# Kernel tuning notes

Hardware: AMD Instinct MI355X
Metric: run time of the kernel (lower is better)

The kernel has to match this reference:

```python
import jax, jax.numpy as jnp
import numpy as np

D_MODEL = 1024
NUM_HEADS = 16
D_HEAD = D_MODEL // NUM_HEADS


def setup_inputs() -> dict:
    key = jax.random.key(0)
    ks = jax.random.split(key, 11)
    B, S = 2, 2048
    s = 1.0 / np.sqrt(D_MODEL)
    inp = {
        "Q": jax.random.normal(ks[0], (B, S, D_MODEL), dtype=jnp.float32),
        "K": jax.random.normal(ks[1], (B, S, D_MODEL), dtype=jnp.float32),
        "V": jax.random.normal(ks[2], (B, S, D_MODEL), dtype=jnp.float32),
        "W_q": jax.random.normal(ks[3], (D_MODEL, D_MODEL), dtype=jnp.float32) * s,
        "b_q": jnp.zeros((D_MODEL,), dtype=jnp.float32),
        "W_k": jax.random.normal(ks[4], (D_MODEL, D_MODEL), dtype=jnp.float32) * s,
        "b_k": jnp.zeros((D_MODEL,), dtype=jnp.float32),
        "W_v": jax.random.normal(ks[5], (D_MODEL, D_MODEL), dtype=jnp.float32) * s,
        "b_v": jnp.zeros((D_MODEL,), dtype=jnp.float32),
        "W_o": jax.random.normal(ks[6], (D_MODEL, D_MODEL), dtype=jnp.float32) * s,
        "b_o": jnp.zeros((D_MODEL,), dtype=jnp.float32),
    }
    return inp


def reference(Q, K, V, W_q, b_q, W_k, b_k, W_v, b_v, W_o, b_o):
    B, S, _ = Q.shape
    # Linear projections (torch Linear: x @ W.T + b)
    q = Q @ W_q.T + b_q  # [B,S,D]
    k = K @ W_k.T + b_k
    v = V @ W_v.T + b_v
    # split heads -> [B,H,S,d]
    q = q.reshape(B, S, NUM_HEADS, D_HEAD).transpose(0, 2, 1, 3)
    k = k.reshape(B, S, NUM_HEADS, D_HEAD).transpose(0, 2, 1, 3)
    v = v.reshape(B, S, NUM_HEADS, D_HEAD).transpose(0, 2, 1, 3)
    scores = jnp.einsum("bhqd,bhkd->bhqk", q, k) / np.sqrt(D_HEAD).astype(np.float32)
    attn = jax.nn.softmax(scores, axis=-1)
    out = jnp.einsum("bhqk,bhkd->bhqd", attn, v)
    out = out.transpose(0, 2, 1, 3).reshape(B, S, D_MODEL)
    return out @ W_o.T + b_o
```

## Files before the change

kernel.cpp:

```cpp
#include <hip/hip_runtime.h>
#include <stdint.h>

#define D_MODEL 1024
#define S_LEN   2048
#define BATCH   2
#define NHEAD   16
#define DHEAD   64
#define NTOK    (BATCH * S_LEN)

typedef unsigned short u16;
typedef __attribute__((ext_vector_type(8))) short bf16x8;
typedef __attribute__((ext_vector_type(4))) float f32x4;
typedef __attribute__((ext_vector_type(16))) float f32x16;
typedef __attribute__((ext_vector_type(2))) unsigned int u32x2;

__device__ __forceinline__ unsigned pack2bf(float lo, float hi) {
    unsigned a = __float_as_uint(lo) + 0x8000u;
    unsigned b = __float_as_uint(hi) + 0x8000u;
    return __builtin_amdgcn_perm(b, a, 0x07060302u);
}
__device__ __forceinline__ u16 f2bf1(float f) {
    return (u16)((__float_as_uint(f) + 0x8000u) >> 16);
}

#define GAS(p) ((const __attribute__((address_space(1))) void*)(p))
#define LAS(p) ((__attribute__((address_space(3))) void*)(p))
#define SWZ8(row, c) (((((row) << 3) | ((c) ^ ((row) & 7)))) << 3)

__global__ __launch_bounds__(256) void convert_kernel(
    const float* __restrict__ Q, const float* __restrict__ K, const float* __restrict__ V,
    const float* __restrict__ Wq, const float* __restrict__ Wk,
    const float* __restrict__ Wv, const float* __restrict__ Wo,
    u16* __restrict__ Qb, u16* __restrict__ Kb, u16* __restrict__ Vb,
    u16* __restrict__ Wqb, u16* __restrict__ Wkb, u16* __restrict__ Wvb, u16* __restrict__ Wob)
{
    const size_t SEG = 262144;
    size_t start = (size_t)blockIdx.x * 4096;
    int s = (int)(start / SEG);
    const float* src; u16* dst; size_t seg0;
    if (s < 4)       { src = Q;  dst = Qb;  seg0 = 0; }
    else if (s < 8)  { src = K;  dst = Kb;  seg0 = 4 * SEG; }
    else if (s < 12) { src = V;  dst = Vb;  seg0 = 8 * SEG; }
    else if (s == 12){ src = Wq; dst = Wqb; seg0 = 12 * SEG; }
    else if (s == 13){ src = Wk; dst = Wkb; seg0 = 13 * SEG; }
    else if (s == 14){ src = Wv; dst = Wvb; seg0 = 14 * SEG; }
    else             { src = Wo; dst = Wob; seg0 = 15 * SEG; }
    size_t off = start - seg0 + threadIdx.x;
    const float4* s4 = (const float4*)src;
    #pragma unroll
    for (int k = 0; k < 16; ++k) {
        float4 x = s4[off + (size_t)k * 256];
        u32x2 p = (u32x2){pack2bf(x.x, x.y), pack2bf(x.z, x.w)};
        *(u32x2*)(dst + (off + (size_t)k * 256) * 4) = p;
    }
}

__global__ __launch_bounds__(512, 2) void proj_kernel(
    const u16* __restrict__ Qb, const u16* __restrict__ Kb, const u16* __restrict__ Vb,
    const u16* __restrict__ Wqb, const u16* __restrict__ Wkb, const u16* __restrict__ Wvb,
    const float* __restrict__ bq, const float* __restrict__ bk, const float* __restrict__ bv,
    u16* __restrict__ qw, u16* __restrict__ kw, u16* __restrict__ vtw)
{
    const int bid = blockIdx.x;
    const int wid = (bid & 7) * 24 + (bid >> 3);
    const int z = wid >> 6;
    const int r = wid & 63;
    const int nbase = (r >> 2) * 256;
    const int mbase = (r & 3) * 256;

    const u16* Ag = (z == 0) ? Wqb : (z == 1) ? Wkb : Wvb;
    const u16* Bg = (z == 0) ? Qb  : (z == 1) ? Kb  : Vb;
    const float* bias = (z == 0) ? bq : (z == 1) ? bk : bv;

    const int tid = threadIdx.x, lane = tid & 63, wave = tid >> 6;
    const int l31 = lane & 31, hh = lane >> 5;
    const int wm = wave >> 2;
    const int wn = wave & 3;

    __shared__ __align__(16) u16 smem[65536];

    size_t aoff[4], boff[4];
    #pragma unroll
    for (int c = 0; c < 4; ++c) {
        int p = (wave * 4 + c) * 64 + lane;
        int row = p >> 3;
        int cg  = (p & 7) ^ (row & 7);
        aoff[c] = (size_t)(mbase + row) * D_MODEL + cg * 8;
        boff[c] = (size_t)(nbase + row) * D_MODEL + cg * 8;
    }

#define STAGE(buf, kc)                                                              \
    do {                                                                            \
        _Pragma("unroll")                                                           \
        for (int c = 0; c < 4; ++c) {                                               \
            __builtin_amdgcn_global_load_lds(GAS(Ag + aoff[c] + (kc)),              \
                LAS(smem + (buf) * 16384 + (wave * 4 + c) * 512), 16, 0, 0);        \
            __builtin_amdgcn_global_load_lds(GAS(Bg + boff[c] + (kc)),              \
                LAS(smem + 32768 + (buf) * 16384 + (wave * 4 + c) * 512), 16, 0, 0);\
        }                                                                           \
    } while (0)

    STAGE(0, 0);

    f32x16 acc[4][2];
    #pragma unroll
    for (int mt = 0; mt < 4; ++mt)
        #pragma unroll
        for (int nt = 0; nt < 2; ++nt)
            #pragma unroll
            for (int q = 0; q < 16; ++q) acc[mt][nt][q] = 0.f;

    for (int t = 0; t < D_MODEL / 64; ++t) {
        const int cur = t & 1;
        asm volatile("s_waitcnt vmcnt(0) lgkmcnt(0)" ::: "memory");
        __builtin_amdgcn_s_barrier();
        asm volatile("" ::: "memory");
        if (t < D_MODEL / 64 - 1) STAGE(cur ^ 1, (t + 1) * 64);
        const u16* Ab = smem + cur * 16384;
        const u16* Bb = smem + 32768 + cur * 16384;
        #pragma unroll
        for (int kk = 0; kk < 4; ++kk) {
            bf16x8 af[4], bfr[2];
            #pragma unroll
            for (int mt = 0; mt < 4; ++mt)
                af[mt] = *(const bf16x8*)&Ab[SWZ8(wm * 128 + mt * 32 + l31, kk * 2 + hh)];
            #pragma unroll
            for (int nt = 0; nt < 2; ++nt)
                bfr[nt] = *(const bf16x8*)&Bb[SWZ8(wn * 64 + nt * 32 + l31, kk * 2 + hh)];
            #pragma unroll
            for (int mt = 0; mt < 4; ++mt)
                #pragma unroll
                for (int nt = 0; nt < 2; ++nt)
                    acc[mt][nt] = __builtin_amdgcn_mfma_f32_32x32x16_bf16(af[mt], bfr[nt], acc[mt][nt], 0, 0, 0);
        }
    }
#undef STAGE

    if (z < 2) {
        u16* Y = z ? kw : qw;
        const float scale = z ? 1.0f : 0.18033688011112042f;
        #pragma unroll
        for (int mt = 0; mt < 4; ++mt)
            #pragma unroll
            for (int nt = 0; nt < 2; ++nt) {
                const int tok = nbase + wn * 64 + nt * 32 + l31;
                u16* yrow = Y + (size_t)tok * D_MODEL;
                #pragma unroll
                for (int g = 0; g < 4; ++g) {
                    const int d0 = mbase + wm * 128 + mt * 32 + 8 * g + 4 * hh;
                    float4 b4 = *(const float4*)&bias[d0];
                    float v0 = (acc[mt][nt][4 * g + 0] + b4.x) * scale;
                    float v1 = (acc[mt][nt][4 * g + 1] + b4.y) * scale;
                    float v2 = (acc[mt][nt][4 * g + 2] + b4.z) * scale;
                    float v3 = (acc[mt][nt][4 * g + 3] + b4.w) * scale;
                    *(u32x2*)(yrow + d0) = (u32x2){pack2bf(v0, v1), pack2bf(v2, v3)};
                }
            }
    } else {
        #pragma unroll
        for (int mt = 0; mt < 4; ++mt)
            #pragma unroll
            for (int nt = 0; nt < 2; ++nt) {
                const int tok = nbase + wn * 64 + nt * 32 + l31;
                #pragma unroll
                for (int g = 0; g < 4; ++g) {
                    const int d0 = mbase + wm * 128 + mt * 32 + 8 * g + 4 * hh;
                    #pragma unroll
                    for (int q = 0; q < 4; ++q)
                        vtw[(size_t)(d0 + q) * NTOK + tok] =
                            f2bf1(acc[mt][nt][4 * g + q] + bias[d0 + q]);
                }
            }
    }
}

__global__ __launch_bounds__(512, 4) void attn_kernel(
    const u16* __restrict__ qw, const u16* __restrict__ kw,
    const u16* __restrict__ vtw, u16* __restrict__ aw)
{
    const int qbase = blockIdx.x * 128;
    const int h = blockIdx.y, b = blockIdx.z;
    const int tid = threadIdx.x, lane = tid & 63, wave = tid >> 6;
    const int wq = wave & 3;
    const int wk = wave >> 2;
    const int l31 = lane & 31;
    const int hh  = lane >> 5;
    const int colbase = h * DHEAD;
    const size_t qrow0 = (size_t)b * S_LEN + qbase;

    __shared__ __align__(16) u16 smem[17664];
    #define KS_OFF(buf) ((buf) * 4096)
    #define VS_OFF(buf) (8192 + (buf) * 4096)

    const int srow = tid >> 3;
    const int scg  = (tid & 7) ^ (srow & 7);
    const size_t ksrc = ((size_t)b * S_LEN + srow) * D_MODEL + colbase + scg * 8;
    const size_t vsrc = (size_t)(colbase + srow) * NTOK + (size_t)b * S_LEN + scg * 8;

    #define STAGE_KV(buf, kv0)                                                         \
        do {                                                                           \
            __builtin_amdgcn_global_load_lds(GAS(kw + ksrc + (size_t)(kv0) * D_MODEL), \
                                             LAS(smem + KS_OFF(buf) + wave * 512), 16, 0, 0); \
            __builtin_amdgcn_global_load_lds(GAS(vtw + vsrc + (kv0)),                  \
                                             LAS(smem + VS_OFF(buf) + wave * 512), 16, 0, 0); \
        } while (0)

    bf16x8 qf[4];
    {
        const u16* qptr = qw + (qrow0 + wq * 32 + l31) * D_MODEL + colbase + hh * 8;
        #pragma unroll
        for (int s = 0; s < 4; ++s) qf[s] = *(const bf16x8*)(qptr + s * 16);
    }

    STAGE_KV(0, 0);

    f32x16 o[2];
    #pragma unroll
    for (int dt = 0; dt < 2; ++dt)
        #pragma unroll
        for (int r = 0; r < 16; ++r) o[dt][r] = 0.f;
    float l = 0.f;

    __syncthreads();

    for (int t = 0; t < S_LEN / 64; ++t) {
        const int cur = t & 1;
        if (t + 1 < S_LEN / 64) STAGE_KV(!cur, (t + 1) * 64);

        f32x16 sc;
        #pragma unroll
        for (int r = 0; r < 16; ++r) sc[r] = -12.f;
        __builtin_amdgcn_s_setprio(1);
        #pragma unroll
        for (int s = 0; s < 4; ++s) {
            bf16x8 kf = *(const bf16x8*)&smem[KS_OFF(cur) + SWZ8(wk * 32 + l31, s * 2 + hh)];
            sc = __builtin_amdgcn_mfma_f32_32x32x16_bf16(kf, qf[s], sc, 0, 0, 0);
        }
        __builtin_amdgcn_s_setprio(0);

        unsigned x[4][2];
        #pragma unroll
        for (int g = 0; g < 4; ++g) {
            float p0 = __builtin_amdgcn_exp2f(sc[4 * g + 0]);
            float p1 = __builtin_amdgcn_exp2f(sc[4 * g + 1]);
            float p2 = __builtin_amdgcn_exp2f(sc[4 * g + 2]);
            float p3 = __builtin_amdgcn_exp2f(sc[4 * g + 3]);
            l += (p0 + p1) + (p2 + p3);
            asm("v_cvt_pk_bf16_f32 %0, %1, %2" : "=v"(x[g][0]) : "v"(p0), "v"(p1));
            asm("v_cvt_pk_bf16_f32 %0, %1, %2" : "=v"(x[g][1]) : "v"(p2), "v"(p3));
        }

        #pragma unroll
        for (int sp = 0; sp < 2; ++sp) {
            unsigned a0 = x[2 * sp][0], b0 = x[2 * sp + 1][0];
            unsigned a1 = x[2 * sp][1], b1 = x[2 * sp + 1][1];
            asm("v_permlane32_swap_b32 %0, %1" : "+v"(a0), "+v"(b0));
            asm("v_permlane32_swap_b32 %0, %1" : "+v"(a1), "+v"(b1));
            union { unsigned u[4]; bf16x8 v; } pf;
            pf.u[0] = a0; pf.u[1] = a1; pf.u[2] = b0; pf.u[3] = b1;
            __builtin_amdgcn_s_setprio(1);
            #pragma unroll
            for (int dt = 0; dt < 2; ++dt) {
                bf16x8 vf = *(const bf16x8*)&smem[VS_OFF(cur) + SWZ8(dt * 32 + l31, wk * 4 + sp * 2 + hh)];
                o[dt] = __builtin_amdgcn_mfma_f32_32x32x16_bf16(vf, pf.v, o[dt], 0, 0, 0);
            }
            __builtin_amdgcn_s_setprio(0);
        }

        __syncthreads();
    }

    l += __shfl_xor(l, 32);

    float* Ored = (float*)smem;
    float* Lred = (float*)(smem + 17408);
    float* op = Ored + ((size_t)wq * 32 + l31) * 68;
    if (wk == 1) {
        #pragma unroll
        for (int dt = 0; dt < 2; ++dt)
            #pragma unroll
            for (int g = 0; g < 4; ++g)
                *(f32x4*)(op + dt * 32 + 8 * g + 4 * hh) =
                    (f32x4){o[dt][4 * g + 0], o[dt][4 * g + 1], o[dt][4 * g + 2], o[dt][4 * g + 3]};
        if (hh == 0) Lred[wq * 32 + l31] = l;
    }
    __syncthreads();
    if (wk == 0) {
        l += Lred[wq * 32 + l31];
        float inv = 1.0f / l;
        size_t orow = (qrow0 + wq * 32 + l31) * D_MODEL + colbase;
        #pragma unroll
        for (int dt = 0; dt < 2; ++dt)
            #pragma unroll
            for (int g = 0; g < 4; ++g) {
                f32x4 add = *(const f32x4*)(op + dt * 32 + 8 * g + 4 * hh);
                float v0 = (o[dt][4 * g + 0] + add[0]) * inv;
                float v1 = (o[dt][4 * g + 1] + add[1]) * inv;
                float v2 = (o[dt][4 * g + 2] + add[2]) * inv;
                float v3 = (o[dt][4 * g + 3] + add[3]) * inv;
                *(u32x2*)(aw + orow + dt * 32 + 8 * g + 4 * hh) =
                    (u32x2){pack2bf(v0, v1), pack2bf(v2, v3)};
            }
    }
    #undef STAGE_KV
    #undef KS_OFF
    #undef VS_OFF
}

__global__ __launch_bounds__(256) void outproj_kernel(
    const u16* __restrict__ aw, const u16* __restrict__ Wob,
    const float* __restrict__ bo, float* __restrict__ out)
{
    const int nbase = blockIdx.x * 64;
    const int mbase = blockIdx.y * 128;
    const int tid = threadIdx.x, lane = tid & 63, wave = tid >> 6;
    const int m16 = lane & 15, quad = lane >> 4;
    const int wm = wave >> 1, wn = wave & 1;

    __shared__ __align__(16) u16 As[128 * 64];
    __shared__ __align__(16) u16 Bs[64 * 64];

    int arow[4], acg[4], brow[2], bcg[2];
    #pragma unroll
    for (int c = 0; c < 4; ++c) {
        int p = (wave * 4 + c) * 64 + lane;
        arow[c] = p >> 3; acg[c] = (p & 7) ^ (arow[c] & 7);
    }
    #pragma unroll
    for (int c = 0; c < 2; ++c) {
        int p = (wave * 2 + c) * 64 + lane;
        brow[c] = p >> 3; bcg[c] = (p & 7) ^ (brow[c] & 7);
    }

    f32x4 acc[4][2];
    #pragma unroll
    for (int mt = 0; mt < 4; ++mt)
        #pragma unroll
        for (int nt = 0; nt < 2; ++nt) acc[mt][nt] = (f32x4){0.f, 0.f, 0.f, 0.f};

    for (int kc = 0; kc < D_MODEL; kc += 64) {
        #pragma unroll
        for (int c = 0; c < 4; ++c)
            __builtin_amdgcn_global_load_lds(
                GAS(Wob + (size_t)(mbase + arow[c]) * D_MODEL + kc + acg[c] * 8),
                LAS(As + (wave * 4 + c) * 512), 16, 0, 0);
        #pragma unroll
        for (int c = 0; c < 2; ++c)
            __builtin_amdgcn_global_load_lds(
                GAS(aw + (size_t)(nbase + brow[c]) * D_MODEL + kc + bcg[c] * 8),
                LAS(Bs + (wave * 2 + c) * 512), 16, 0, 0);
        __syncthreads();
        #pragma unroll
        for (int half = 0; half < 2; ++half) {
            bf16x8 af[4], bfr[2];
            #pragma unroll
            for (int mt = 0; mt < 4; ++mt)
                af[mt] = *(const bf16x8*)&As[SWZ8(wm * 64 + mt * 16 + m16, quad + 4 * half)];
            #pragma unroll
            for (int nt = 0; nt < 2; ++nt)
                bfr[nt] = *(const bf16x8*)&Bs[SWZ8(wn * 32 + nt * 16 + m16, quad + 4 * half)];
            #pragma unroll
            for (int mt = 0; mt < 4; ++mt)
                #pragma unroll
                for (int nt = 0; nt < 2; ++nt)
                    acc[mt][nt] = __builtin_amdgcn_mfma_f32_16x16x32_bf16(af[mt], bfr[nt], acc[mt][nt], 0, 0, 0);
        }
        __syncthreads();
    }

    #pragma unroll
    for (int mt = 0; mt < 4; ++mt) {
        int d0 = mbase + wm * 64 + mt * 16 + quad * 4;
        float4 b4 = *(const float4*)&bo[d0];
        #pragma unroll
        for (int nt = 0; nt < 2; ++nt) {
            int tok = nbase + wn * 32 + nt * 16 + m16;
            float4 st;
            st.x = acc[mt][nt][0] + b4.x;
            st.y = acc[mt][nt][1] + b4.y;
            st.z = acc[mt][nt][2] + b4.z;
            st.w = acc[mt][nt][3] + b4.w;
            *(float4*)(out + (size_t)tok * D_MODEL + d0) = st;
        }
    }
}

extern "C" void kernel_launch(void* const* d_in, const int* in_sizes, int n_in,
                              void* d_out, int out_size, void* d_ws, size_t ws_size,
                              hipStream_t stream) {
    const float* Q  = (const float*)d_in[0];
    const float* K  = (const float*)d_in[1];
    const float* V  = (const float*)d_in[2];
    const float* Wq = (const float*)d_in[3];
    const float* bq = (const float*)d_in[4];
    const float* Wk = (const float*)d_in[5];
    const float* bk = (const float*)d_in[6];
    const float* Wv = (const float*)d_in[7];
    const float* bv = (const float*)d_in[8];
    const float* Wo = (const float*)d_in[9];
    const float* bo = (const float*)d_in[10];

    const size_t NT = (size_t)NTOK * D_MODEL;
    const size_t WN = (size_t)D_MODEL * D_MODEL;
    u16* base = (u16*)d_ws;
    u16* qw  = base;
    u16* kw  = base + NT;
    u16* vtw = base + 2 * NT;
    u16* Qb  = base + 3 * NT;
    u16* Kb  = base + 4 * NT;
    u16* Vb  = base + 5 * NT;
    u16* Wqb = base + 6 * NT;
    u16* Wkb = Wqb + WN;
    u16* Wvb = Wkb + WN;
    u16* Wob = Wvb + WN;
    u16* aww = Qb;

    convert_kernel<<<1024, 256, 0, stream>>>(Q, K, V, Wq, Wk, Wv, Wo,
                                             Qb, Kb, Vb, Wqb, Wkb, Wvb, Wob);
    proj_kernel<<<dim3(192), 512, 0, stream>>>(Qb, Kb, Vb, Wqb, Wkb, Wvb,
                                               bq, bk, bv, qw, kw, vtw);
    attn_kernel<<<dim3(S_LEN / 128, NHEAD, BATCH), 512, 0, stream>>>(qw, kw, vtw, aww);
    outproj_kernel<<<dim3(NTOK / 64, D_MODEL / 128), 256, 0, stream>>>(
        aww, Wob, bo, (float*)d_out);
}
```

Before: 214.0 us.

## Restructure projection GEMM main loop into barrier-synchronized quadrant phases with MFMA priority

The projection GEMM's K-loop now splits each 64-wide k-tile into four quadrant phases. Each phase loads A/B fragments from LDS for all four k-steps and then runs MFMAs on a 2x1 sub-block of the accumulator tile. Barriers around each MFMA burst and s_setprio(1) are meant to interleave waves so one wave's LDS reads overlap another's MFMA work, ping-pong style. The prefetch of the next tile is issued in the first phase and waited on only in the last, which keeps global loads in flight longer. The cost is two extra workgroup barriers per phase and more fragment registers, so occupancy could drop.

```diff
diff --git a/kernel.cpp b/kernel.cpp
--- a/kernel.cpp
+++ b/kernel.cpp
@@ -110,28 +110,38 @@
             #pragma unroll
             for (int q = 0; q < 16; ++q) acc[mt][nt][q] = 0.f;
 
-    for (int t = 0; t < D_MODEL / 64; ++t) {
+    asm volatile("s_waitcnt vmcnt(0)" ::: "memory");
+    __builtin_amdgcn_s_barrier();
+    asm volatile("" ::: "memory");
+
+    for (int t = 0; t < 16; ++t) {
         const int cur = t & 1;
-        asm volatile("s_waitcnt vmcnt(0) lgkmcnt(0)" ::: "memory");
-        __builtin_amdgcn_s_barrier();
-        asm volatile("" ::: "memory");
-        if (t < D_MODEL / 64 - 1) STAGE(cur ^ 1, (t + 1) * 64);
         const u16* Ab = smem + cur * 16384;
         const u16* Bb = smem + 32768 + cur * 16384;
         #pragma unroll
-        for (int kk = 0; kk < 4; ++kk) {
-            bf16x8 af[4], bfr[2];
-            #pragma unroll
-            for (int mt = 0; mt < 4; ++mt)
-                af[mt] = *(const bf16x8*)&Ab[SWZ8(wm * 128 + mt * 32 + l31, kk * 2 + hh)];
-            #pragma unroll
-            for (int nt = 0; nt < 2; ++nt)
-                bfr[nt] = *(const bf16x8*)&Bb[SWZ8(wn * 64 + nt * 32 + l31, kk * 2 + hh)];
-            #pragma unroll
-            for (int mt = 0; mt < 4; ++mt)
-                #pragma unroll
-                for (int nt = 0; nt < 2; ++nt)
-                    acc[mt][nt] = __builtin_amdgcn_mfma_f32_32x32x16_bf16(af[mt], bfr[nt], acc[mt][nt], 0, 0, 0);
+        for (int q = 0; q < 4; ++q) {
+            const int qm = q >> 1, qn = q & 1;
+            if (q == 0 && t < 15) STAGE(cur ^ 1, (t + 1) * 64);
+            bf16x8 af0[4], af1[4], bfr[4];
+            #pragma unroll
+            for (int kk = 0; kk < 4; ++kk) {
+                af0[kk] = *(const bf16x8*)&Ab[SWZ8(wm * 128 + (2 * qm) * 32 + l31, kk * 2 + hh)];
+                af1[kk] = *(const bf16x8*)&Ab[SWZ8(wm * 128 + (2 * qm + 1) * 32 + l31, kk * 2 + hh)];
+                bfr[kk] = *(const bf16x8*)&Bb[SWZ8(wn * 64 + qn * 32 + l31, kk * 2 + hh)];
+            }
+            if (q == 3 && t < 15) asm volatile("s_waitcnt vmcnt(0)" ::: "memory");
+            asm volatile("" ::: "memory");
+            __builtin_amdgcn_s_barrier();
+            asm volatile("s_waitcnt lgkmcnt(0)" ::: "memory");
+            __builtin_amdgcn_s_setprio(1);
+            #pragma unroll
+            for (int kk = 0; kk < 4; ++kk) {
+                acc[2 * qm][qn]     = __builtin_amdgcn_mfma_f32_32x32x16_bf16(af0[kk], bfr[kk], acc[2 * qm][qn], 0, 0, 0);
+                acc[2 * qm + 1][qn] = __builtin_amdgcn_mfma_f32_32x32x16_bf16(af1[kk], bfr[kk], acc[2 * qm + 1][qn], 0, 0, 0);
+            }
+            __builtin_amdgcn_s_setprio(0);
+            asm volatile("" ::: "memory");
+            __builtin_amdgcn_s_barrier();
         }
     }
 #undef STAGE
```

Result: slower. 226.2 us (+5.7%).

## Rework output projection into double-buffered 128x128 tiles using 32x32 MFMA

Applied to the files above, without the earlier changes.

The output-projection GEMM now uses 128x128 tiles with 512 threads and 256 blocks remapped in a swizzled order. Global-to-LDS loads are double-buffered so the next K chunk is fetched while the current one is computed. The inner product switches from 16x16x32 to 32x32x16 MFMA instructions with raised scheduling priority. The aim is to hide load latency, raise data reuse per block and cut barriers, at the cost of fewer blocks and more LDS per block.

```diff
diff --git a/kernel.cpp b/kernel.cpp
--- a/kernel.cpp
+++ b/kernel.cpp
@@ -307,82 +307,90 @@
     #undef VS_OFF
 }
 
-__global__ __launch_bounds__(256) void outproj_kernel(
+__global__ __launch_bounds__(512, 2) void outproj_kernel(
     const u16* __restrict__ aw, const u16* __restrict__ Wob,
     const float* __restrict__ bo, float* __restrict__ out)
 {
-    const int nbase = blockIdx.x * 64;
-    const int mbase = blockIdx.y * 128;
+    const int bid = blockIdx.x;
+    const int wid = (bid & 7) * 32 + (bid >> 3);
+    const int mbase = (wid & 7) * 128;
+    const int nbase = (wid >> 3) * 128;
+
     const int tid = threadIdx.x, lane = tid & 63, wave = tid >> 6;
-    const int m16 = lane & 15, quad = lane >> 4;
-    const int wm = wave >> 1, wn = wave & 1;
-
-    __shared__ __align__(16) u16 As[128 * 64];
-    __shared__ __align__(16) u16 Bs[64 * 64];
-
-    int arow[4], acg[4], brow[2], bcg[2];
-    #pragma unroll
-    for (int c = 0; c < 4; ++c) {
-        int p = (wave * 4 + c) * 64 + lane;
-        arow[c] = p >> 3; acg[c] = (p & 7) ^ (arow[c] & 7);
-    }
+    const int l31 = lane & 31, hh = lane >> 5;
+    const int wm = wave >> 2;
+    const int wn = wave & 3;
+
+    __shared__ __align__(16) u16 smem[32768];
+
+    size_t aoff[2], boff[2];
     #pragma unroll
     for (int c = 0; c < 2; ++c) {
-        int p = (wave * 2 + c) * 64 + lane;
-        brow[c] = p >> 3; bcg[c] = (p & 7) ^ (brow[c] & 7);
-    }
-
-    f32x4 acc[4][2];
-    #pragma unroll
-    for (int mt = 0; mt < 4; ++mt)
-        #pragma unroll
-        for (int nt = 0; nt < 2; ++nt) acc[mt][nt] = (f32x4){0.f, 0.f, 0.f, 0.f};
-
-    for (int kc = 0; kc < D_MODEL; kc += 64) {
-        #pragma unroll
-        for (int c = 0; c < 4; ++c)
-            __builtin_amdgcn_global_load_lds(
-                GAS(Wob + (size_t)(mbase + arow[c]) * D_MODEL + kc + acg[c] * 8),
-                LAS(As + (wave * 4 + c) * 512), 16, 0, 0);
-        #pragma unroll
-        for (int c = 0; c < 2; ++c)
-            __builtin_amdgcn_global_load_lds(
-                GAS(aw + (size_t)(nbase + brow[c]) * D_MODEL + kc + bcg[c] * 8),
-                LAS(Bs + (wave * 2 + c) * 512), 16, 0, 0);
-        __syncthreads();
-        #pragma unroll
-        for (int half = 0; half < 2; ++half) {
-            bf16x8 af[4], bfr[2];
-            #pragma unroll
-            for (int mt = 0; mt < 4; ++mt)
-                af[mt] = *(const bf16x8*)&As[SWZ8(wm * 64 + mt * 16 + m16, quad + 4 * half)];
-            #pragma unroll
-            for (int nt = 0; nt < 2; ++nt)
-                bfr[nt] = *(const bf16x8*)&Bs[SWZ8(wn * 32 + nt * 16 + m16, quad + 4 * half)];
-            #pragma unroll
-            for (int mt = 0; mt < 4; ++mt)
-                #pragma unroll
-                for (int nt = 0; nt < 2; ++nt)
-                    acc[mt][nt] = __builtin_amdgcn_mfma_f32_16x16x32_bf16(af[mt], bfr[nt], acc[mt][nt], 0, 0, 0);
-        }
-        __syncthreads();
-    }
-
-    #pragma unroll
-    for (int mt = 0; mt < 4; ++mt) {
-        int d0 = mbase + wm * 64 + mt * 16 + quad * 4;
-        float4 b4 = *(const float4*)&bo[d0];
-        #pragma unroll
-        for (int nt = 0; nt < 2; ++nt) {
-            int tok = nbase + wn * 32 + nt * 16 + m16;
+        int p = c * 512 + tid;
+        int row = p >> 3;
+        int cg  = (p & 7) ^ (row & 7);
+        aoff[c] = (size_t)(mbase + row) * D_MODEL + cg * 8;
+        boff[c] = (size_t)(nbase + row) * D_MODEL + cg * 8;
+    }
+
+#define OSTAGE(buf, kc)                                                             \
+    do {                                                                            \
+        _Pragma("unroll")                                                           \
+        for (int c = 0; c < 2; ++c) {                                               \
+            __builtin_amdgcn_global_load_lds(GAS(Wob + aoff[c] + (kc)),             \
+                LAS(smem + (buf) * 8192 + c * 4096 + wave * 512), 16, 0, 0);        \
+            __builtin_amdgcn_global_load_lds(GAS(aw + boff[c] + (kc)),              \
+                LAS(smem + 16384 + (buf) * 8192 + c * 4096 + wave * 512), 16, 0, 0);\
+        }                                                                           \
+    } while (0)
+
+    OSTAGE(0, 0);
+
+    f32x16 acc[2];
+    #pragma unroll
+    for (int mt = 0; mt < 2; ++mt)
+        #pragma unroll
+        for (int q = 0; q < 16; ++q) acc[mt][q] = 0.f;
+
+    for (int t = 0; t < D_MODEL / 64; ++t) {
+        const int cur = t & 1;
+        asm volatile("s_waitcnt vmcnt(0) lgkmcnt(0)" ::: "memory");
+        __builtin_amdgcn_s_barrier();
+        asm volatile("" ::: "memory");
+        if (t < D_MODEL / 64 - 1) OSTAGE(cur ^ 1, (t + 1) * 64);
+        const u16* Ab = smem + cur * 8192;
+        const u16* Bb = smem + 16384 + cur * 8192;
+        #pragma unroll
+        for (int kk = 0; kk < 4; ++kk) {
+            bf16x8 af[2], bfr;
+            #pragma unroll
+            for (int mt = 0; mt < 2; ++mt)
+                af[mt] = *(const bf16x8*)&Ab[SWZ8(wm * 64 + mt * 32 + l31, kk * 2 + hh)];
+            bfr = *(const bf16x8*)&Bb[SWZ8(wn * 32 + l31, kk * 2 + hh)];
+            __builtin_amdgcn_s_setprio(1);
+            #pragma unroll
+            for (int mt = 0; mt < 2; ++mt)
+                acc[mt] = __builtin_amdgcn_mfma_f32_32x32x16_bf16(af[mt], bfr, acc[mt], 0, 0, 0);
+            __builtin_amdgcn_s_setprio(0);
+        }
+    }
+#undef OSTAGE
+
+    const int tok = nbase + wn * 32 + l31;
+    float* orow = out + (size_t)tok * D_MODEL;
+    #pragma unroll
+    for (int mt = 0; mt < 2; ++mt)
+        #pragma unroll
+        for (int g = 0; g < 4; ++g) {
+            const int d0 = mbase + wm * 64 + mt * 32 + 8 * g + 4 * hh;
+            float4 b4 = *(const float4*)&bo[d0];
             float4 st;
-            st.x = acc[mt][nt][0] + b4.x;
-            st.y = acc[mt][nt][1] + b4.y;
-            st.z = acc[mt][nt][2] + b4.z;
-            st.w = acc[mt][nt][3] + b4.w;
-            *(float4*)(out + (size_t)tok * D_MODEL + d0) = st;
-        }
-    }
+            st.x = acc[mt][4 * g + 0] + b4.x;
+            st.y = acc[mt][4 * g + 1] + b4.y;
+            st.z = acc[mt][4 * g + 2] + b4.z;
+            st.w = acc[mt][4 * g + 3] + b4.w;
+            *(float4*)(orow + d0) = st;
+        }
 }
 
 extern "C" void kernel_launch(void* const* d_in, const int* in_sizes, int n_in,
@@ -420,6 +428,5 @@
     proj_kernel<<<dim3(192), 512, 0, stream>>>(Qb, Kb, Vb, Wqb, Wkb, Wvb,
                                                bq, bk, bv, qw, kw, vtw);
     attn_kernel<<<dim3(S_LEN / 128, NHEAD, BATCH), 512, 0, stream>>>(qw, kw, vtw, aww);
-    outproj_kernel<<<dim3(NTOK / 64, D_MODEL / 128), 256, 0, stream>>>(
-        aww, Wob, bo, (float*)d_out);
-}
+    outproj_kernel<<<dim3(256), 512, 0, stream>>>(aww, Wob, bo, (float*)d_out);
+}
```

New measurement: 212.3 us. No clear change (-0.8%).
